# Optimization experiments

Hardware: AMD Instinct MI355X
Metric: run time of the kernel (lower is better)

Reference implementation:

```python
import jax, jax.numpy as jnp
import numpy as np

L = 5        # num GNN layers
H = 256      # hidden size
N = 200000   # total nodes in batch
E = 400000   # total edges
G = 8000     # number of graphs (25 nodes each)


def _gelu(x):
    return jax.nn.gelu(x, approximate=False)


def _ln(x, g, b, eps=1e-5):
    m = x.mean(-1, keepdims=True)
    v = ((x - m) ** 2).mean(-1, keepdims=True)
    return (x - m) / jnp.sqrt(v + eps) * g + b


def _mlp(x, w1, b1, g, bb, w2, b2):
    # Linear -> LayerNorm -> GELU -> Linear (dropout is identity in eval)
    h = x @ w1 + b1
    h = _ln(h, g, bb)
    h = _gelu(h)
    return h @ w2 + b2


def setup_inputs() -> dict:
    key = jax.random.key(0)
    ks = jax.random.split(key, 24)
    s = 0.02
    inp = {}
    inp['x'] = jax.random.randint(ks[0], (N,), 0, 118)
    inp['edge_index'] = jax.random.randint(ks[1], (2, E), 0, N)
    inp['edge_attr'] = jax.random.randint(ks[2], (E,), 0, 5)
    # deterministic sorted graph ids: 25 nodes per graph, all G graphs nonempty
    inp['batch'] = jnp.arange(N, dtype=jnp.int32) // (N // G)
    # embeddings
    inp['atom_emb'] = jax.random.normal(ks[3], (118, H), jnp.float32) * s
    inp['vn_emb'] = jnp.zeros((1, H), jnp.float32)  # init constant 0
    inp['bond_emb'] = jax.random.normal(ks[4], (L, 5, H), jnp.float32) * s
    inp['eps'] = jnp.zeros((L,), jnp.float32)
    # GINConv mlp params (stacked over layers)
    inp['c_w1'] = jax.random.normal(ks[5], (L, H, 4 * H), jnp.float32) * s
    inp['c_b1'] = jnp.zeros((L, 4 * H), jnp.float32)
    inp['c_lng'] = jnp.ones((L, 4 * H), jnp.float32)
    inp['c_lnb'] = jnp.zeros((L, 4 * H), jnp.float32)
    inp['c_w2'] = jax.random.normal(ks[6], (L, 4 * H, H), jnp.float32) * s
    inp['c_b2'] = jnp.zeros((L, H), jnp.float32)
    # per-layer output LayerNorms
    inp['n_g'] = jnp.ones((L, H), jnp.float32)
    inp['n_b'] = jnp.zeros((L, H), jnp.float32)
    # virtual-node MLPs (L-1 of them)
    inp['v_w1'] = jax.random.normal(ks[7], (L - 1, H, 4 * H), jnp.float32) * s
    inp['v_b1'] = jnp.zeros((L - 1, 4 * H), jnp.float32)
    inp['v_lng'] = jnp.ones((L - 1, 4 * H), jnp.float32)
    inp['v_lnb'] = jnp.zeros((L - 1, 4 * H), jnp.float32)
    inp['v_w2'] = jax.random.normal(ks[8], (L - 1, 4 * H, H), jnp.float32) * s
    inp['v_b2'] = jnp.zeros((L - 1, H), jnp.float32)
    # projection head
    inp['p_w1'] = jax.random.normal(ks[9], (H, H), jnp.float32) * s
    inp['p_b1'] = jnp.zeros((H,), jnp.float32)
    inp['p_lng'] = jnp.ones((H,), jnp.float32)
    inp['p_lnb'] = jnp.zeros((H,), jnp.float32)
    inp['p_w2'] = jax.random.normal(ks[10], (H, H), jnp.float32) * s
    inp['p_b2'] = jnp.zeros((H,), jnp.float32)
    return inp


def reference(x, edge_index, edge_attr, batch, atom_emb, vn_emb, bond_emb, eps,
              c_w1, c_b1, c_lng, c_lnb, c_w2, c_b2, n_g, n_b,
              v_w1, v_b1, v_lng, v_lnb, v_w2, v_b2,
              p_w1, p_b1, p_lng, p_lnb, p_w2, p_b2):
    src, dst = edge_index[0], edge_index[1]
    vn = jnp.broadcast_to(vn_emb[0], (G, H))  # virtualnode embedding per graph
    h = atom_emb[x]                            # [N, H]
    for l in range(L):
        h = h + vn[batch]
        h_in = h
        # GINConv: gather + add + gelu per edge, scatter-add at dst
        edge_e = bond_emb[l][edge_attr]        # [E, H]
        msg = _gelu(h[src] + edge_e)           # [E, H]
        aggr = jax.ops.segment_sum(msg, dst, num_segments=N)
        out = _mlp((1.0 + eps[l]) * h + aggr,
                   c_w1[l], c_b1[l], c_lng[l], c_lnb[l], c_w2[l], c_b2[l])
        out = _ln(out, n_g[l], n_b[l])
        if l < L - 1:
            out = _gelu(out)
        h = out + h_in                         # residual
        if l < L - 1:
            vp = jax.ops.segment_max(h_in, batch, num_segments=G)
            vn = vn + _mlp(vp, v_w1[l], v_b1[l], v_lng[l], v_lnb[l], v_w2[l], v_b2[l])
    h_graph = jax.ops.segment_sum(h, batch, num_segments=G)  # [G, H]
    z = h_graph @ p_w1 + p_b1
    z = _gelu(_ln(z, p_lng, p_lnb))
    z = z @ p_w2 + p_b2
    z = z / jnp.linalg.norm(z, axis=-1, keepdims=True)
    return z
```

## Files before the change

### kernel.cpp

```cpp
#include <hip/hip_runtime.h>
#include <math.h>

typedef __bf16 bf16_t;
typedef __bf16 bfrag  __attribute__((ext_vector_type(8)));
typedef __bf16 b4     __attribute__((ext_vector_type(4)));
typedef __bf16 b2v    __attribute__((ext_vector_type(2)));
typedef float  f32x4  __attribute__((ext_vector_type(4)));

static constexpr int LY  = 5;
static constexpr int H   = 256;
static constexpr int NN  = 200000;
static constexpr int EE  = 400000;
static constexpr int GG  = 8000;
static constexpr int NPG = 25;
static constexpr int CAP = 24;
static constexpr int NBLK_NODE = NN / 32;
static constexpr int NBLK_VN   = GG / 32;

__device__ __forceinline__ float gelu_f(float x) {
    const float y = 0.7978845608028654f * x * (1.0f + 0.044715f * x * x);
    const float e = __expf(2.0f * y);
    const float t = 1.0f - 2.0f / (e + 1.0f);
    return 0.5f * x * (1.0f + t);
}

__global__ void k_fill(float* __restrict__ out, float v, int n) {
    const int i = blockIdx.x * 256 + threadIdx.x;
    if (i < n) out[i] = v;
}

__global__ void k_detect(const void* __restrict__ probe, int* __restrict__ flag) {
    const bf16_t* p = (const bf16_t*)probe;
    int bad = 0;
    for (int i = threadIdx.x; i < 256; i += 64) {
        const float v = (float)p[i];
        if (!(v == v) || fabsf(v) > 1000.0f) bad = 1;
    }
    const int any = __any(bad) ? 1 : 0;
    if (threadIdx.x == 0) *flag = any;
}

struct CvtJobs {
    const void* src[18];
    bf16_t*     dst[18];
    int         pfx[19];
    int         njobs;
};
__global__ void k_cvt_all(CvtJobs J, const int* __restrict__ flag) {
    const int i = blockIdx.x * 256 + threadIdx.x;
    if (i >= J.pfx[J.njobs]) return;
    int j = 0;
    while (i >= J.pfx[j + 1]) ++j;
    const int loc = i - J.pfx[j];
    if (*flag) J.dst[j][loc] = (bf16_t)((const float*)J.src[j])[loc];
    else       J.dst[j][loc] = ((const bf16_t*)J.src[j])[loc];
}

struct TpJobs {
    const void* s32[22];
    const void* s16[22];
    bf16_t*     dst[22];
    int R[22], C[22];
    int pfx[23];
    int njobs;
};
__global__ void k_tp_all(TpJobs J, const int* __restrict__ flag) {
    __shared__ bf16_t t[32][33];
    const int tile = blockIdx.x;
    int j = 0;
    while (tile >= J.pfx[j + 1]) ++j;
    const int tl = tile - J.pfx[j];
    const int C = J.C[j], R = J.R[j];
    const int ntx = C / 32;
    const int c0 = (tl % ntx) * 32, r0 = (tl / ntx) * 32;
    const int f = *flag;
    const int tx = threadIdx.x & 31, ty = threadIdx.x >> 5;
    #pragma unroll
    for (int i = 0; i < 4; ++i) {
        const int r = ty + i * 8;
        const size_t idx = (size_t)(r0 + r) * C + c0 + tx;
        t[r][tx] = f ? (bf16_t)((const float*)J.s32[j])[idx] : ((const bf16_t*)J.s16[j])[idx];
    }
    __syncthreads();
    #pragma unroll
    for (int i = 0; i < 4; ++i) {
        const int r = ty + i * 8;
        J.dst[j][(size_t)(c0 + r) * R + r0 + tx] = t[tx][r];
    }
}

__global__ void k_init_h(const int* __restrict__ x, const bf16_t* __restrict__ atom,
                         bf16_t* __restrict__ h) {
    const size_t idx = (size_t)blockIdx.x * 256 + threadIdx.x;
    const int row = (int)(idx >> 8), col = (int)(idx & 255);
    h[idx] = atom[(size_t)x[row] * H + col];
}

__global__ void k_init_vn(const bf16_t* __restrict__ vne, float* __restrict__ vn) {
    const size_t idx = (size_t)blockIdx.x * 256 + threadIdx.x;
    vn[idx] = (float)vne[idx & 255];
}

__global__ void k_zero_cnt(int* __restrict__ cnt) {
    const int i = blockIdx.x * 256 + threadIdx.x;
    if (i < NN) cnt[i] = 0;
}

__global__ void k_bucket(const int* __restrict__ ei, const int* __restrict__ ea,
                         int* __restrict__ cnt, int* __restrict__ slots) {
    const int e = blockIdx.x * 256 + threadIdx.x;
    if (e >= EE) return;
    const int d = ei[EE + e];
    const int s = ei[e];
    const int a = ea[e];
    const int slot = atomicAdd(&cnt[d], 1);
    if (slot < CAP) slots[(size_t)d * CAP + slot] = s | (a << 18);
}

__global__ void k_addvn_segmax(bf16_t* __restrict__ h, const float* __restrict__ vn,
                               bf16_t* __restrict__ vp, int do_max) {
    const int g = blockIdx.x, t = threadIdx.x;
    const float2 v = *(const float2*)(vn + (size_t)g * H + 2 * t);
    float mx0 = -1e30f, mx1 = -1e30f;
    #pragma unroll 5
    for (int i = 0; i < NPG; ++i) {
        bf16_t* p = h + ((size_t)g * NPG + i) * H + 2 * t;
        const b2v hv = *(const b2v*)p;
        const float h0 = (float)hv[0] + v.x;
        const float h1 = (float)hv[1] + v.y;
        b2v o; o[0] = (bf16_t)h0; o[1] = (bf16_t)h1;
        *(b2v*)p = o;
        mx0 = fmaxf(mx0, h0); mx1 = fmaxf(mx1, h1);
    }
    if (do_max) {
        b2v o; o[0] = (bf16_t)mx0; o[1] = (bf16_t)mx1;
        *(b2v*)(vp + (size_t)g * H + 2 * t) = o;
    }
}

__global__ void k_gather(const bf16_t* __restrict__ h,
                         const bf16_t* __restrict__ bondl,
                         const int* __restrict__ cnt, const int* __restrict__ slots,
                         const bf16_t* __restrict__ epsb, int l, bf16_t* __restrict__ Xb) {
    const int n = blockIdx.x, t = threadIdx.x;
    int deg = cnt[n];
    if (deg > CAP) deg = CAP;
    float m0 = 0.0f, m1 = 0.0f;
    for (int i = 0; i < deg; ++i) {
        const int p = slots[(size_t)n * CAP + i];
        const int s = p & 0x3FFFF;
        const int a = p >> 18;
        const b2v hv = *(const b2v*)(h + (size_t)s * H + 2 * t);
        const b2v bv = *(const b2v*)(bondl + (size_t)a * H + 2 * t);
        m0 += gelu_f((float)hv[0] + (float)bv[0]);
        m1 += gelu_f((float)hv[1] + (float)bv[1]);
    }
    const float eps1 = 1.0f + (float)epsb[l];
    const b2v hn = *(const b2v*)(h + (size_t)n * H + 2 * t);
    b2v o;
    o[0] = (bf16_t)(eps1 * (float)hn[0] + m0);
    o[1] = (bf16_t)(eps1 * (float)hn[1] + m1);
    *(b2v*)(Xb + (size_t)n * H + 2 * t) = o;
}

__global__ void k_graphsum(const bf16_t* __restrict__ h, bf16_t* __restrict__ hg) {
    const int g = blockIdx.x, t = threadIdx.x;
    float s0 = 0.0f, s1 = 0.0f;
    #pragma unroll 5
    for (int i = 0; i < NPG; ++i) {
        const b2v hv = *(const b2v*)(h + ((size_t)g * NPG + i) * H + 2 * t);
        s0 += (float)hv[0]; s1 += (float)hv[1];
    }
    b2v o; o[0] = (bf16_t)s0; o[1] = (bf16_t)s1;
    *(b2v*)(hg + (size_t)g * H + 2 * t) = o;
}

__global__ void k_norm(const float* __restrict__ z, float* __restrict__ out) {
    const int row = blockIdx.x, t = threadIdx.x;
    const size_t idx = (size_t)row * H + t;
    const float v = z[idx];
    float q = v * v;
    #pragma unroll
    for (int o = 32; o > 0; o >>= 1) q += __shfl_xor(q, o, 64);
    __shared__ float rq[4];
    const int wave = t >> 6, lane = t & 63;
    if (lane == 0) rq[wave] = q;
    __syncthreads();
    q = rq[0] + rq[1] + rq[2] + rq[3];
    out[idx] = v * rsqrtf(q);
}

__launch_bounds__(512, 4)
__global__ void k_mlp_dual(const bf16_t* __restrict__ Xn, const bf16_t* __restrict__ Xv,
                           const bf16_t* __restrict__ nW1T, const bf16_t* __restrict__ vW1T,
                           const bf16_t* __restrict__ nb1, const bf16_t* __restrict__ vb1,
                           const bf16_t* __restrict__ nlng, const bf16_t* __restrict__ vlng,
                           const bf16_t* __restrict__ nlnb, const bf16_t* __restrict__ vlnb,
                           const bf16_t* __restrict__ nW2T, const bf16_t* __restrict__ vW2T,
                           const bf16_t* __restrict__ nb2, const bf16_t* __restrict__ vb2,
                           const bf16_t* __restrict__ g2, const bf16_t* __restrict__ b2ln,
                           bf16_t* __restrict__ hres, float* __restrict__ vnacc,
                           int gelu_flag, int nblk_node, int has_vn) {
    constexpr int HID = 1024;
    constexpr int NP1 = HID / 128;
    constexpr int NQ2 = HID / 64;
    __shared__ bf16_t hid[32 * HID];
    __shared__ bf16_t wbuf[8192];
    const int tid  = threadIdx.x;
    const int lane = tid & 63, wave = tid >> 6;
    const int c16  = lane & 15, quad = lane >> 4;

    const bool is_node = (int)blockIdx.x < nblk_node;
    const size_t rowblk = is_node ? (size_t)blockIdx.x * 32
                                  : (size_t)((int)blockIdx.x - nblk_node) * 32;
    const bf16_t* X    = is_node ? Xn   : Xv;
    const bf16_t* W1T  = is_node ? nW1T : vW1T;
    const bf16_t* W2T  = is_node ? nW2T : vW2T;
    const bf16_t* b1   = is_node ? nb1  : vb1;
    const bf16_t* lng  = is_node ? nlng : vlng;
    const bf16_t* lnb  = is_node ? nlnb : vlnb;
    const bf16_t* b2   = is_node ? nb2  : vb2;

    auto stage = [&](const bf16_t* WT, int KW, int colbase, int k0) {
        #pragma unroll
        for (int j = 0; j < 2; ++j) {
            const int grp    = wave * 2 + j;
            const int colrel = grp * 8 + (lane >> 3);
            const int slot   = lane & 7;
            const int kq     = slot ^ (colrel & 7);
            const bf16_t* gp = WT + (size_t)(colbase + colrel) * KW + k0 + kq * 8;
            bf16_t* lp = &wbuf[(size_t)grp * 512];
            __builtin_amdgcn_global_load_lds(
                (const __attribute__((address_space(1))) void*)gp,
                (__attribute__((address_space(3))) void*)lp, 16, 0, 0);
        }
    };
    auto wfrag = [&](int crel, int g) -> bfrag {
        return *(const bfrag*)(wbuf + crel * 64 + ((g ^ (crel & 7)) * 8));
    };

    const bf16_t* xr0 = X + (rowblk + c16) * 256 + quad * 8;
    const bf16_t* xr1 = X + (rowblk + 16 + c16) * 256 + quad * 8;
    bfrag xa[8][2];
    #pragma unroll
    for (int ks = 0; ks < 8; ++ks) {
        xa[ks][0] = *(const bfrag*)(xr0 + ks * 32);
        xa[ks][1] = *(const bfrag*)(xr1 + ks * 32);
    }

    #pragma unroll
    for (int c = 0; c < NP1; ++c) {
        const int nbase = c * 128 + wave * 16;
        f32x4 acc[2];
        acc[0] = f32x4{0.f, 0.f, 0.f, 0.f};
        acc[1] = f32x4{0.f, 0.f, 0.f, 0.f};
        #pragma unroll
        for (int kc = 0; kc < 4; ++kc) {
            stage(W1T, 256, c * 128, kc * 64);
            __syncthreads();
            #pragma unroll
            for (int s = 0; s < 2; ++s) {
                const int ks = kc * 2 + s;
                const int g  = s * 4 + quad;
                const bfrag w0 = wfrag(wave * 16 + c16, g);
                #pragma unroll
                for (int mt = 0; mt < 2; ++mt)
                    acc[mt] = __builtin_amdgcn_mfma_f32_16x16x32_bf16(
                        w0, xa[ks][mt], acc[mt], 0, 0, 0);
            }
            __syncthreads();
        }
        #pragma unroll
        for (int mt = 0; mt < 2; ++mt) {
            const int kb = nbase + quad * 4;
            const int xr = mt * 16 + c16;
            const b4 bias = *(const b4*)(b1 + kb);
            b4 o;
            #pragma unroll
            for (int r = 0; r < 4; ++r)
                o[r] = (bf16_t)(acc[mt][r] + (float)bias[r]);
            const int ch = ((kb >> 3) ^ (xr & 7));
            *(b4*)(hid + xr * HID + ch * 8 + (kb & 7)) = o;
        }
    }
    __syncthreads();

    {
        const int row = tid >> 4, p = tid & 15;
        float sum = 0.f, ss = 0.f;
        #pragma unroll
        for (int i = 0; i < HID / 128; ++i) {
            const int j0 = p * 8 + i * 128;
            const int ch = ((j0 >> 3) ^ (row & 7));
            bfrag v = *(const bfrag*)(hid + row * HID + ch * 8);
            #pragma unroll
            for (int k = 0; k < 8; ++k) { const float f = (float)v[k]; sum += f; ss += f * f; }
        }
        #pragma unroll
        for (int o = 1; o < 16; o <<= 1) { sum += __shfl_xor(sum, o, 64); ss += __shfl_xor(ss, o, 64); }
        const float mean = sum * (1.0f / HID);
        const float var  = ss * (1.0f / HID) - mean * mean;
        const float rinv = rsqrtf(var + 1e-5f);
        #pragma unroll
        for (int i = 0; i < HID / 128; ++i) {
            const int j0 = p * 8 + i * 128;
            const int ch = ((j0 >> 3) ^ (row & 7));
            bfrag v  = *(const bfrag*)(hid + row * HID + ch * 8);
            bfrag gv = *(const bfrag*)(lng + j0);
            bfrag bv = *(const bfrag*)(lnb + j0);
            bfrag o8;
            #pragma unroll
            for (int k = 0; k < 8; ++k) {
                const float f = ((float)v[k] - mean) * rinv * (float)gv[k] + (float)bv[k];
                o8[k] = (bf16_t)gelu_f(f);
            }
            *(bfrag*)(hid + row * HID + ch * 8) = o8;
        }
    }
    __syncthreads();

    {
        f32x4 acc2[2][2];
        #pragma unroll
        for (int cp = 0; cp < 2; ++cp)
            #pragma unroll
            for (int mt = 0; mt < 2; ++mt)
                acc2[cp][mt] = f32x4{0.f, 0.f, 0.f, 0.f};
        #pragma unroll
        for (int cp = 0; cp < 2; ++cp) {
            for (int q2 = 0; q2 < NQ2; ++q2) {
                stage(W2T, HID, cp * 128, q2 * 64);
                __syncthreads();
                #pragma unroll
                for (int s = 0; s < 2; ++s) {
                    const int g = s * 4 + quad;
                    const bfrag w0 = wfrag(wave * 16 + c16, g);
                    const int k = q2 * 64 + s * 32 + quad * 8;
                    bfrag hb[2];
                    #pragma unroll
                    for (int mt = 0; mt < 2; ++mt) {
                        const int row = mt * 16 + c16;
                        const int ch = ((k >> 3) ^ (row & 7));
                        hb[mt] = *(const bfrag*)(hid + row * HID + ch * 8);
                    }
                    #pragma unroll
                    for (int mt = 0; mt < 2; ++mt)
                        acc2[cp][mt] = __builtin_amdgcn_mfma_f32_16x16x32_bf16(
                            w0, hb[mt], acc2[cp][mt], 0, 0, 0);
                }
                __syncthreads();
            }
        }

        if (!is_node) {
            if (has_vn) {
                #pragma unroll
                for (int cp = 0; cp < 2; ++cp)
                    #pragma unroll
                    for (int mt = 0; mt < 2; ++mt) {
                        const int cb = cp * 128 + wave * 16 + quad * 4;
                        const b4 b2vv = *(const b4*)(b2 + cb);
                        float* po = vnacc + (rowblk + mt * 16 + c16) * 256 + cb;
                        const f32x4 old = *(const f32x4*)po;
                        f32x4 v;
                        #pragma unroll
                        for (int r = 0; r < 4; ++r) v[r] = old[r] + acc2[cp][mt][r] + (float)b2vv[r];
                        *(f32x4*)po = v;
                    }
            }
        } else {
            constexpr int OS = 260;
            float* ot = (float*)hid;
            __syncthreads();
            #pragma unroll
            for (int cp = 0; cp < 2; ++cp)
                #pragma unroll
                for (int mt = 0; mt < 2; ++mt) {
                    const int cb = cp * 128 + wave * 16 + quad * 4;
                    const b4 b2vv = *(const b4*)(b2 + cb);
                    f32x4 v;
                    #pragma unroll
                    for (int r = 0; r < 4; ++r) v[r] = acc2[cp][mt][r] + (float)b2vv[r];
                    *(f32x4*)(ot + (mt * 16 + c16) * OS + cb) = v;
                }
            __syncthreads();
            const int row = tid >> 4, p = tid & 15;
            float s = 0.f, q = 0.f;
            #pragma unroll
            for (int i = 0; i < 16; ++i) {
                const float f = ot[row * OS + p + 16 * i];
                s += f; q += f * f;
            }
            #pragma unroll
            for (int o = 1; o < 16; o <<= 1) { s += __shfl_xor(s, o, 64); q += __shfl_xor(q, o, 64); }
            const float mean = s * (1.0f / 256.0f);
            const float var  = q * (1.0f / 256.0f) - mean * mean;
            const float rinv = rsqrtf(var + 1e-5f);
            const size_t rg = (rowblk + row) * 256;
            #pragma unroll
            for (int i = 0; i < 2; ++i) {
                const int j0 = p * 16 + i * 8;
                bfrag gv = *(const bfrag*)(g2 + j0);
                bfrag bv = *(const bfrag*)(b2ln + j0);
                bfrag hv = *(const bfrag*)(hres + rg + j0);
                bfrag o8;
                #pragma unroll
                for (int k = 0; k < 8; ++k) {
                    float f = (ot[row * OS + j0 + k] - mean) * rinv * (float)gv[k] + (float)bv[k];
                    if (gelu_flag) f = gelu_f(f);
                    o8[k] = (bf16_t)(f + (float)hv[k]);
                }
                *(bfrag*)(hres + rg + j0) = o8;
            }
        }
    }
}

__launch_bounds__(512, 4)
__global__ void k_mlp_proj(const bf16_t* __restrict__ X, const bf16_t* __restrict__ W1T,
                           const bf16_t* __restrict__ b1, const bf16_t* __restrict__ lng,
                           const bf16_t* __restrict__ lnb, const bf16_t* __restrict__ W2T,
                           const bf16_t* __restrict__ b2, float* __restrict__ outf) {
    constexpr int HID = 256;
    constexpr int NP1 = HID / 128;
    constexpr int NQ2 = HID / 64;
    __shared__ bf16_t hid[32 * HID];
    __shared__ bf16_t wbuf[8192];
    const int tid  = threadIdx.x;
    const int lane = tid & 63, wave = tid >> 6;
    const int c16  = lane & 15, quad = lane >> 4;
    const size_t rowblk = (size_t)blockIdx.x * 32;

    auto stage = [&](const bf16_t* WT, int KW, int colbase, int k0) {
        #pragma unroll
        for (int j = 0; j < 2; ++j) {
            const int grp    = wave * 2 + j;
            const int colrel = grp * 8 + (lane >> 3);
            const int slot   = lane & 7;
            const int kq     = slot ^ (colrel & 7);
            const bf16_t* gp = WT + (size_t)(colbase + colrel) * KW + k0 + kq * 8;
            bf16_t* lp = &wbuf[(size_t)grp * 512];
            __builtin_amdgcn_global_load_lds(
                (const __attribute__((address_space(1))) void*)gp,
                (__attribute__((address_space(3))) void*)lp, 16, 0, 0);
        }
    };
    auto wfrag = [&](int crel, int g) -> bfrag {
        return *(const bfrag*)(wbuf + crel * 64 + ((g ^ (crel & 7)) * 8));
    };

    const bf16_t* xr0 = X + (rowblk + c16) * 256 + quad * 8;
    const bf16_t* xr1 = X + (rowblk + 16 + c16) * 256 + quad * 8;
    bfrag xa[8][2];
    #pragma unroll
    for (int ks = 0; ks < 8; ++ks) {
        xa[ks][0] = *(const bfrag*)(xr0 + ks * 32);
        xa[ks][1] = *(const bfrag*)(xr1 + ks * 32);
    }

    #pragma unroll
    for (int c = 0; c < NP1; ++c) {
        const int nbase = c * 128 + wave * 16;
        f32x4 acc[2];
        acc[0] = f32x4{0.f, 0.f, 0.f, 0.f};
        acc[1] = f32x4{0.f, 0.f, 0.f, 0.f};
        #pragma unroll
        for (int kc = 0; kc < 4; ++kc) {
            stage(W1T, 256, c * 128, kc * 64);
            __syncthreads();
            #pragma unroll
            for (int s = 0; s < 2; ++s) {
                const int ks = kc * 2 + s;
                const int g  = s * 4 + quad;
                const bfrag w0 = wfrag(wave * 16 + c16, g);
                #pragma unroll
                for (int mt = 0; mt < 2; ++mt)
                    acc[mt] = __builtin_amdgcn_mfma_f32_16x16x32_bf16(
                        w0, xa[ks][mt], acc[mt], 0, 0, 0);
            }
            __syncthreads();
        }
        #pragma unroll
        for (int mt = 0; mt < 2; ++mt) {
            const int kb = nbase + quad * 4;
            const int xr = mt * 16 + c16;
            const b4 bias = *(const b4*)(b1 + kb);
            b4 o;
            #pragma unroll
            for (int r = 0; r < 4; ++r)
                o[r] = (bf16_t)(acc[mt][r] + (float)bias[r]);
            const int ch = ((kb >> 3) ^ (xr & 7));
            *(b4*)(hid + xr * HID + ch * 8 + (kb & 7)) = o;
        }
    }
    __syncthreads();

    {
        const int row = tid >> 4, p = tid & 15;
        float sum = 0.f, ss = 0.f;
        #pragma unroll
        for (int i = 0; i < HID / 128; ++i) {
            const int j0 = p * 8 + i * 128;
            const int ch = ((j0 >> 3) ^ (row & 7));
            bfrag v = *(const bfrag*)(hid + row * HID + ch * 8);
            #pragma unroll
            for (int k = 0; k < 8; ++k) { const float f = (float)v[k]; sum += f; ss += f * f; }
        }
        #pragma unroll
        for (int o = 1; o < 16; o <<= 1) { sum += __shfl_xor(sum, o, 64); ss += __shfl_xor(ss, o, 64); }
        const float mean = sum * (1.0f / HID);
        const float var  = ss * (1.0f / HID) - mean * mean;
        const float rinv = rsqrtf(var + 1e-5f);
        #pragma unroll
        for (int i = 0; i < HID / 128; ++i) {
            const int j0 = p * 8 + i * 128;
            const int ch = ((j0 >> 3) ^ (row & 7));
            bfrag v  = *(const bfrag*)(hid + row * HID + ch * 8);
            bfrag gv = *(const bfrag*)(lng + j0);
            bfrag bv = *(const bfrag*)(lnb + j0);
            bfrag o8;
            #pragma unroll
            for (int k = 0; k < 8; ++k) {
                const float f = ((float)v[k] - mean) * rinv * (float)gv[k] + (float)bv[k];
                o8[k] = (bf16_t)gelu_f(f);
            }
            *(bfrag*)(hid + row * HID + ch * 8) = o8;
        }
    }
    __syncthreads();

    {
        f32x4 acc2[2][2];
        #pragma unroll
        for (int cp = 0; cp < 2; ++cp)
            #pragma unroll
            for (int mt = 0; mt < 2; ++mt)
                acc2[cp][mt] = f32x4{0.f, 0.f, 0.f, 0.f};
        #pragma unroll
        for (int cp = 0; cp < 2; ++cp) {
            for (int q2 = 0; q2 < NQ2; ++q2) {
                stage(W2T, HID, cp * 128, q2 * 64);
                __syncthreads();
                #pragma unroll
                for (int s = 0; s < 2; ++s) {
                    const int g = s * 4 + quad;
                    const bfrag w0 = wfrag(wave * 16 + c16, g);
                    const int k = q2 * 64 + s * 32 + quad * 8;
                    bfrag hb[2];
                    #pragma unroll
                    for (int mt = 0; mt < 2; ++mt) {
                        const int row = mt * 16 + c16;
                        const int ch = ((k >> 3) ^ (row & 7));
                        hb[mt] = *(const bfrag*)(hid + row * HID + ch * 8);
                    }
                    #pragma unroll
                    for (int mt = 0; mt < 2; ++mt)
                        acc2[cp][mt] = __builtin_amdgcn_mfma_f32_16x16x32_bf16(
                            w0, hb[mt], acc2[cp][mt], 0, 0, 0);
                }
                __syncthreads();
            }
        }
        #pragma unroll
        for (int cp = 0; cp < 2; ++cp)
            #pragma unroll
            for (int mt = 0; mt < 2; ++mt) {
                const int cb = cp * 128 + wave * 16 + quad * 4;
                const b4 b2vv = *(const b4*)(b2 + cb);
                f32x4 v;
                #pragma unroll
                for (int r = 0; r < 4; ++r) v[r] = acc2[cp][mt][r] + (float)b2vv[r];
                *(f32x4*)(outf + (rowblk + mt * 16 + c16) * 256 + cb) = v;
            }
    }
}

extern "C" void kernel_launch(void* const* d_in, const int* in_sizes, int n_in,
                              void* d_out, int out_size, void* d_ws, size_t ws_size,
                              hipStream_t stream) {
    float* outz = (float*)d_out;

    const bool layout_ok =
        (n_in == 28) &&
        in_sizes[0] == 200000 && in_sizes[1] == 800000 &&
        in_sizes[2] == 400000 && in_sizes[3] == 200000 &&
        in_sizes[4] == 118 * 256 && in_sizes[6] == 5 * 5 * 256 &&
        in_sizes[8] == 5 * 256 * 1024 && in_sizes[27] == 256 &&
        out_size == GG * H;
    if (!layout_ok) {
        k_fill<<<(out_size + 255) / 256, 256, 0, stream>>>(outz, 777.0f, out_size);
        return;
    }

    char* w = (char*)d_ws;
    size_t off = 0;
    auto alloc = [&](size_t bytes) -> void* {
        void* p = w + off;
        off += (bytes + 255) & ~(size_t)255;
        return p;
    };
    bf16_t* h     = (bf16_t*)alloc((size_t)NN * H * 2);
    bf16_t* Xb    = (bf16_t*)alloc((size_t)NN * H * 2);
    float*  vn    = (float*) alloc((size_t)GG * H * 4);
    bf16_t* vpb   = (bf16_t*)alloc((size_t)GG * H * 2);
    bf16_t* hgb   = (bf16_t*)alloc((size_t)GG * H * 2);
    float*  pout2 = (float*) alloc((size_t)GG * H * 4);
    int*    cnt   = (int*)   alloc((size_t)NN * 4);
    int*    slots = (int*)   alloc((size_t)NN * CAP * 4);
    int*    dflag = (int*)   alloc(256);
    bf16_t* cw1T  = (bf16_t*)alloc((size_t)LY * 1024 * 256 * 2);
    bf16_t* cw2T  = (bf16_t*)alloc((size_t)LY * 256 * 1024 * 2);
    bf16_t* vw1T  = (bf16_t*)alloc((size_t)(LY - 1) * 1024 * 256 * 2);
    bf16_t* vw2T  = (bf16_t*)alloc((size_t)(LY - 1) * 256 * 1024 * 2);
    bf16_t* pw1T  = (bf16_t*)alloc((size_t)256 * 256 * 2);
    bf16_t* pw2T  = (bf16_t*)alloc((size_t)256 * 256 * 2);
    bf16_t* atomA = (bf16_t*)alloc((size_t)118 * 256 * 2);
    bf16_t* vneA  = (bf16_t*)alloc(256 * 2);
    bf16_t* bondA = (bf16_t*)alloc((size_t)LY * 5 * 256 * 2);
    bf16_t* epsA  = (bf16_t*)alloc(16 * 2);
    bf16_t* cb1A  = (bf16_t*)alloc((size_t)LY * 1024 * 2);
    bf16_t* clngA = (bf16_t*)alloc((size_t)LY * 1024 * 2);
    bf16_t* clnbA = (bf16_t*)alloc((size_t)LY * 1024 * 2);
    bf16_t* cb2A  = (bf16_t*)alloc((size_t)LY * 256 * 2);
    bf16_t* ngA   = (bf16_t*)alloc((size_t)LY * 256 * 2);
    bf16_t* nbA   = (bf16_t*)alloc((size_t)LY * 256 * 2);
    bf16_t* vb1A  = (bf16_t*)alloc((size_t)(LY - 1) * 1024 * 2);
    bf16_t* vlngA = (bf16_t*)alloc((size_t)(LY - 1) * 1024 * 2);
    bf16_t* vlnbA = (bf16_t*)alloc((size_t)(LY - 1) * 1024 * 2);
    bf16_t* vb2A  = (bf16_t*)alloc((size_t)(LY - 1) * 256 * 2);
    bf16_t* pb1A  = (bf16_t*)alloc(256 * 2);
    bf16_t* plngA = (bf16_t*)alloc(256 * 2);
    bf16_t* plnbA = (bf16_t*)alloc(256 * 2);
    bf16_t* pb2A  = (bf16_t*)alloc(256 * 2);
    if (off > ws_size) {
        k_fill<<<(out_size + 255) / 256, 256, 0, stream>>>(outz, 333.0f, out_size);
        return;
    }

    const int* xi  = (const int*)d_in[0];
    const int* ei  = (const int*)d_in[1];
    const int* ea  = (const int*)d_in[2];

    k_detect<<<1, 64, 0, stream>>>(d_in[8], dflag);

    {
        CvtJobs J{};
        struct { int idx; bf16_t* dst; int n; } cj[18] = {
            {4, atomA, 118 * 256}, {5, vneA, 256}, {6, bondA, LY * 5 * 256}, {7, epsA, LY},
            {9, cb1A, LY * 1024}, {10, clngA, LY * 1024}, {11, clnbA, LY * 1024},
            {13, cb2A, LY * 256}, {14, ngA, LY * 256}, {15, nbA, LY * 256},
            {17, vb1A, (LY - 1) * 1024}, {18, vlngA, (LY - 1) * 1024},
            {19, vlnbA, (LY - 1) * 1024}, {21, vb2A, (LY - 1) * 256},
            {23, pb1A, 256}, {24, plngA, 256}, {25, plnbA, 256}, {27, pb2A, 256},
        };
        int acc = 0;
        J.njobs = 18;
        for (int j = 0; j < 18; ++j) {
            J.src[j] = d_in[cj[j].idx];
            J.dst[j] = cj[j].dst;
            J.pfx[j] = acc;
            acc += cj[j].n;
        }
        J.pfx[18] = acc;
        k_cvt_all<<<(acc + 255) / 256, 256, 0, stream>>>(J, dflag);
    }

    {
        TpJobs J{};
        int nj = 0, acc = 0;
        auto add = [&](int idx, size_t eoff, bf16_t* dst, int R, int C) {
            J.s32[nj] = (const void*)((const float*) d_in[idx] + eoff);
            J.s16[nj] = (const void*)((const bf16_t*)d_in[idx] + eoff);
            J.dst[nj] = dst; J.R[nj] = R; J.C[nj] = C;
            J.pfx[nj] = acc;
            acc += (C / 32) * (R / 32);
            ++nj;
        };
        for (int l = 0; l < LY; ++l) {
            add(8,  (size_t)l * 256 * 1024, cw1T + (size_t)l * 1024 * 256, 256, 1024);
            add(12, (size_t)l * 1024 * 256, cw2T + (size_t)l * 256 * 1024, 1024, 256);
        }
        for (int l = 0; l < LY - 1; ++l) {
            add(16, (size_t)l * 256 * 1024, vw1T + (size_t)l * 1024 * 256, 256, 1024);
            add(20, (size_t)l * 1024 * 256, vw2T + (size_t)l * 256 * 1024, 1024, 256);
        }
        add(22, 0, pw1T, 256, 256);
        add(26, 0, pw2T, 256, 256);
        J.pfx[nj] = acc;
        J.njobs = nj;
        k_tp_all<<<acc, 256, 0, stream>>>(J, dflag);
    }

    k_init_h<<<NN, 256, 0, stream>>>(xi, atomA, h);
    k_init_vn<<<GG, 256, 0, stream>>>(vneA, vn);
    k_zero_cnt<<<(NN + 255) / 256, 256, 0, stream>>>(cnt);
    k_bucket<<<(EE + 255) / 256, 256, 0, stream>>>(ei, ea, cnt, slots);

    for (int l = 0; l < LY; ++l) {
        const int has_vn = (l < LY - 1) ? 1 : 0;
        k_addvn_segmax<<<GG, 128, 0, stream>>>(h, vn, vpb, has_vn);
        k_gather<<<NN, 128, 0, stream>>>(h, bondA + (size_t)l * 5 * H,
                                         cnt, slots, epsA, l, Xb);
        const int lv = (l < LY - 1) ? l : 0;
        k_mlp_dual<<<NBLK_NODE + (has_vn ? NBLK_VN : 0), 512, 0, stream>>>(
            Xb, vpb,
            cw1T + (size_t)l * 1024 * 256, vw1T + (size_t)lv * 1024 * 256,
            cb1A + (size_t)l * 1024,       vb1A + (size_t)lv * 1024,
            clngA + (size_t)l * 1024,      vlngA + (size_t)lv * 1024,
            clnbA + (size_t)l * 1024,      vlnbA + (size_t)lv * 1024,
            cw2T + (size_t)l * 256 * 1024, vw2T + (size_t)lv * 256 * 1024,
            cb2A + (size_t)l * 256,        vb2A + (size_t)lv * 256,
            ngA + (size_t)l * H, nbA + (size_t)l * H,
            h, vn, has_vn, NBLK_NODE, has_vn);
    }

    k_graphsum<<<GG, 128, 0, stream>>>(h, hgb);
    k_mlp_proj<<<GG / 32, 512, 0, stream>>>(hgb, pw1T, pb1A, plngA, plnbA, pw2T, pb2A, pout2);
    k_norm<<<GG, 256, 0, stream>>>(pout2, outz);
}
```

Baseline: 4.093 ms.

## Enlarge MLP row tile to 64 rows with 16 waves sharing staged weights

The fused node/virtual-node MLP kernel now processes 64 rows per block instead of 32, using 1024 threads split into two row groups of 8 column waves. Each weight tile staged into LDS is reused by both row groups, which halves weight traffic per row and halves the block count. In exchange, LDS use per block grows to about 144KB, so only one block fits per CU. Every block-wide barrier now synchronises 16 waves, which may add stall time.

```diff
diff --git a/kernel.cpp b/kernel.cpp
--- a/kernel.cpp
+++ b/kernel.cpp
@@ -14,8 +14,9 @@
 static constexpr int GG  = 8000;
 static constexpr int NPG = 25;
 static constexpr int CAP = 24;
-static constexpr int NBLK_NODE = NN / 32;
-static constexpr int NBLK_VN   = GG / 32;
+static constexpr int MROW = 64;
+static constexpr int NBLK_NODE = NN / MROW;
+static constexpr int NBLK_VN   = GG / MROW;
 
 __device__ __forceinline__ float gelu_f(float x) {
     const float y = 0.7978845608028654f * x * (1.0f + 0.044715f * x * x);
@@ -190,7 +191,7 @@
     out[idx] = v * rsqrtf(q);
 }
 
-__launch_bounds__(512, 4)
+__launch_bounds__(1024, 4)
 __global__ void k_mlp_dual(const bf16_t* __restrict__ Xn, const bf16_t* __restrict__ Xv,
                            const bf16_t* __restrict__ nW1T, const bf16_t* __restrict__ vW1T,
                            const bf16_t* __restrict__ nb1, const bf16_t* __restrict__ vb1,
@@ -202,17 +203,17 @@
                            bf16_t* __restrict__ hres, float* __restrict__ vnacc,
                            int gelu_flag, int nblk_node, int has_vn) {
     constexpr int HID = 1024;
-    constexpr int NP1 = HID / 128;
-    constexpr int NQ2 = HID / 64;
-    __shared__ bf16_t hid[32 * HID];
-    __shared__ bf16_t wbuf[8192];
+    __shared__ __align__(16) bf16_t hid[MROW * HID];
+    __shared__ __align__(16) bf16_t wbuf[8192];
     const int tid  = threadIdx.x;
     const int lane = tid & 63, wave = tid >> 6;
     const int c16  = lane & 15, quad = lane >> 4;
+    const int wcol = wave & 7;
+    const int wrow = wave >> 3;
 
     const bool is_node = (int)blockIdx.x < nblk_node;
-    const size_t rowblk = is_node ? (size_t)blockIdx.x * 32
-                                  : (size_t)((int)blockIdx.x - nblk_node) * 32;
+    const size_t rowblk = is_node ? (size_t)blockIdx.x * MROW
+                                  : (size_t)((int)blockIdx.x - nblk_node) * MROW;
     const bf16_t* X    = is_node ? Xn   : Xv;
     const bf16_t* W1T  = is_node ? nW1T : vW1T;
     const bf16_t* W2T  = is_node ? nW2T : vW2T;
@@ -222,25 +223,22 @@
     const bf16_t* b2   = is_node ? nb2  : vb2;
 
     auto stage = [&](const bf16_t* WT, int KW, int colbase, int k0) {
-        #pragma unroll
-        for (int j = 0; j < 2; ++j) {
-            const int grp    = wave * 2 + j;
-            const int colrel = grp * 8 + (lane >> 3);
-            const int slot   = lane & 7;
-            const int kq     = slot ^ (colrel & 7);
-            const bf16_t* gp = WT + (size_t)(colbase + colrel) * KW + k0 + kq * 8;
-            bf16_t* lp = &wbuf[(size_t)grp * 512];
-            __builtin_amdgcn_global_load_lds(
-                (const __attribute__((address_space(1))) void*)gp,
-                (__attribute__((address_space(3))) void*)lp, 16, 0, 0);
-        }
+        const int grp    = wave;
+        const int colrel = grp * 8 + (lane >> 3);
+        const int slot   = lane & 7;
+        const int kq     = slot ^ (colrel & 7);
+        const bf16_t* gp = WT + (size_t)(colbase + colrel) * KW + k0 + kq * 8;
+        bf16_t* lp = &wbuf[(size_t)grp * 512];
+        __builtin_amdgcn_global_load_lds(
+            (const __attribute__((address_space(1))) void*)gp,
+            (__attribute__((address_space(3))) void*)lp, 16, 0, 0);
     };
     auto wfrag = [&](int crel, int g) -> bfrag {
         return *(const bfrag*)(wbuf + crel * 64 + ((g ^ (crel & 7)) * 8));
     };
 
-    const bf16_t* xr0 = X + (rowblk + c16) * 256 + quad * 8;
-    const bf16_t* xr1 = X + (rowblk + 16 + c16) * 256 + quad * 8;
+    const bf16_t* xr0 = X + (rowblk + wrow * 32 + c16) * 256 + quad * 8;
+    const bf16_t* xr1 = X + (rowblk + wrow * 32 + 16 + c16) * 256 + quad * 8;
     bfrag xa[8][2];
     #pragma unroll
     for (int ks = 0; ks < 8; ++ks) {
@@ -249,8 +247,8 @@
     }
 
     #pragma unroll
-    for (int c = 0; c < NP1; ++c) {
-        const int nbase = c * 128 + wave * 16;
+    for (int c = 0; c < 8; ++c) {
+        const int nbase = c * 128 + wcol * 16;
         f32x4 acc[2];
         acc[0] = f32x4{0.f, 0.f, 0.f, 0.f};
         acc[1] = f32x4{0.f, 0.f, 0.f, 0.f};
@@ -262,7 +260,7 @@
             for (int s = 0; s < 2; ++s) {
                 const int ks = kc * 2 + s;
                 const int g  = s * 4 + quad;
-                const bfrag w0 = wfrag(wave * 16 + c16, g);
+                const bfrag w0 = wfrag(wcol * 16 + c16, g);
                 #pragma unroll
                 for (int mt = 0; mt < 2; ++mt)
                     acc[mt] = __builtin_amdgcn_mfma_f32_16x16x32_bf16(
@@ -273,7 +271,7 @@
         #pragma unroll
         for (int mt = 0; mt < 2; ++mt) {
             const int kb = nbase + quad * 4;
-            const int xr = mt * 16 + c16;
+            const int xr = wrow * 32 + mt * 16 + c16;
             const b4 bias = *(const b4*)(b1 + kb);
             b4 o;
             #pragma unroll
@@ -328,18 +326,18 @@
                 acc2[cp][mt] = f32x4{0.f, 0.f, 0.f, 0.f};
         #pragma unroll
         for (int cp = 0; cp < 2; ++cp) {
-            for (int q2 = 0; q2 < NQ2; ++q2) {
+            for (int q2 = 0; q2 < 16; ++q2) {
                 stage(W2T, HID, cp * 128, q2 * 64);
                 __syncthreads();
                 #pragma unroll
                 for (int s = 0; s < 2; ++s) {
                     const int g = s * 4 + quad;
-                    const bfrag w0 = wfrag(wave * 16 + c16, g);
+                    const bfrag w0 = wfrag(wcol * 16 + c16, g);
                     const int k = q2 * 64 + s * 32 + quad * 8;
                     bfrag hb[2];
                     #pragma unroll
                     for (int mt = 0; mt < 2; ++mt) {
-                        const int row = mt * 16 + c16;
+                        const int row = wrow * 32 + mt * 16 + c16;
                         const int ch = ((k >> 3) ^ (row & 7));
                         hb[mt] = *(const bfrag*)(hid + row * HID + ch * 8);
                     }
@@ -358,9 +356,9 @@
                 for (int cp = 0; cp < 2; ++cp)
                     #pragma unroll
                     for (int mt = 0; mt < 2; ++mt) {
-                        const int cb = cp * 128 + wave * 16 + quad * 4;
+                        const int cb = cp * 128 + wcol * 16 + quad * 4;
                         const b4 b2vv = *(const b4*)(b2 + cb);
-                        float* po = vnacc + (rowblk + mt * 16 + c16) * 256 + cb;
+                        float* po = vnacc + (rowblk + wrow * 32 + mt * 16 + c16) * 256 + cb;
                         const f32x4 old = *(const f32x4*)po;
                         f32x4 v;
                         #pragma unroll
@@ -376,12 +374,12 @@
             for (int cp = 0; cp < 2; ++cp)
                 #pragma unroll
                 for (int mt = 0; mt < 2; ++mt) {
-                    const int cb = cp * 128 + wave * 16 + quad * 4;
+                    const int cb = cp * 128 + wcol * 16 + quad * 4;
                     const b4 b2vv = *(const b4*)(b2 + cb);
                     f32x4 v;
                     #pragma unroll
                     for (int r = 0; r < 4; ++r) v[r] = acc2[cp][mt][r] + (float)b2vv[r];
-                    *(f32x4*)(ot + (mt * 16 + c16) * OS + cb) = v;
+                    *(f32x4*)(ot + (wrow * 32 + mt * 16 + c16) * OS + cb) = v;
                 }
             __syncthreads();
             const int row = tid >> 4, p = tid & 15;
@@ -702,7 +700,7 @@
         k_gather<<<NN, 128, 0, stream>>>(h, bondA + (size_t)l * 5 * H,
                                          cnt, slots, epsA, l, Xb);
         const int lv = (l < LY - 1) ? l : 0;
-        k_mlp_dual<<<NBLK_NODE + (has_vn ? NBLK_VN : 0), 512, 0, stream>>>(
+        k_mlp_dual<<<NBLK_NODE + (has_vn ? NBLK_VN : 0), 1024, 0, stream>>>(
             Xb, vpb,
             cw1T + (size_t)l * 1024 * 256, vw1T + (size_t)lv * 1024 * 256,
             cb1A + (size_t)l * 1024,       vb1A + (size_t)lv * 1024,
```

New measurement: 4.630 ms. +13.1%, slower.
